# Kernel optimization log

Hardware: AMD Instinct MI355X
Metric: run time of the kernel (lower is better)

## Reference

```python
import jax, jax.numpy as jnp
import numpy as np
import math

NUM_HEADS = 8

def setup_inputs() -> dict:
    key = jax.random.key(0)
    k1, k2, k3 = jax.random.split(key, 3)
    B, N, C = 16, 4096, 512
    x = jax.random.normal(k1, (B, N, C), dtype=jnp.float32)
    qkv_w = jax.random.normal(k2, (3 * C, C), dtype=jnp.float32) * 0.02
    proj_w = jax.random.normal(k3, (C, C), dtype=jnp.float32) * 0.02
    proj_b = jnp.zeros((C,), dtype=jnp.float32)
    return {"x": x, "qkv_w": qkv_w, "proj_w": proj_w, "proj_b": proj_b}


def reference(x, qkv_w, proj_w, proj_b):
    # Attention with is_mask=1: row-wise windowed attention.
    B, N, C = x.shape
    H = W = int(math.isqrt(N))
    nh = NUM_HEADS
    hd = C // nh
    scale = hd ** (-0.5)

    # fold rows into batch: (B*H, W, C)
    img = x.reshape(B * H, W, C)
    # qkv linear (no bias): (B*H, W, 3C) -> (3, B*H, nh, W, hd)
    qkv = jnp.einsum('bwc,dc->bwd', img, qkv_w)
    qkv = qkv.reshape(B * H, W, 3, nh, hd).transpose(2, 0, 3, 1, 4)
    q, k, v = qkv[0], qkv[1], qkv[2]

    # scaled dot-product attention within each row window
    attn = jnp.einsum('bhqd,bhkd->bhqk', q, k) * scale
    attn = jax.nn.softmax(attn, axis=-1)
    out = jnp.einsum('bhqk,bhkd->bhqd', attn, v)   # (B*H, nh, W, hd)
    out = out.transpose(0, 2, 1, 3).reshape(B, N, C)

    # output projection
    return jnp.einsum('bnc,dc->bnd', out, proj_w) + proj_b
```

## Files before the change

### kernel.cpp

```cpp
#include <hip/hip_runtime.h>
#include <cstdint>
#include <cstddef>

typedef _Float16 half8 __attribute__((ext_vector_type(8)));
typedef _Float16 half4 __attribute__((ext_vector_type(4)));
typedef float f32x4 __attribute__((ext_vector_type(4)));

#define GLDS16(g, l) __builtin_amdgcn_global_load_lds( \
    (__attribute__((address_space(1))) void*)(g), \
    (__attribute__((address_space(3))) void*)(l), 16, 0, 0)

__global__ __launch_bounds__(256) void cvt_f32_f16(const float* __restrict__ src,
                                                   _Float16* __restrict__ dst, int n) {
  int i = (blockIdx.x * 256 + threadIdx.x) * 8;
  if (i >= n) return;
  float4 a = *(const float4*)(src + i);
  float4 b = *(const float4*)(src + i + 4);
  half8 h;
  h[0] = (_Float16)a.x; h[1] = (_Float16)a.y; h[2] = (_Float16)a.z; h[3] = (_Float16)a.w;
  h[4] = (_Float16)b.x; h[5] = (_Float16)b.y; h[6] = (_Float16)b.z; h[7] = (_Float16)b.w;
  *(half8*)(dst + i) = h;
}

template<int NOUT, int NT, bool BIAS>
__global__ __launch_bounds__(512, 2) void gemm_bt(const _Float16* __restrict__ A,
                                                  const _Float16* __restrict__ Bw,
                                                  const float* __restrict__ bias,
                                                  void* __restrict__ Cout) {
  constexpr int K = 512;
  constexpr int NIT = K / 32;
  __shared__ union {
    _Float16 S[3][2][8192];
    float E[2][16][264];
  } u;
  const int id  = blockIdx.x;
  const int xcd = id & 7;
  const int jj  = id >> 3;
  const int by  = (jj / NT) * 8 + xcd;
  const int bx  = jj % NT;
  const int m_base = by * 256, n_base = bx * 256;

  const int t    = threadIdx.x;
  const int lane = t & 63;
  const int wid  = t >> 6;
  const int wm   = wid & 1;
  const int wn   = wid >> 1;
  const int cl   = lane & 15, q = lane >> 4;

  f32x4 acc[8][4] = {};

  const int s0 = t, s1 = t + 512;
  const int r0 = ((s0 >> 6) << 4) | (s0 & 15), c0 = (s0 >> 4) & 3;
  const int r1 = ((s1 >> 6) << 4) | (s1 & 15), c1 = (s1 >> 4) & 3;
  const _Float16* a0 = A  + (size_t)(m_base + r0) * K + c0 * 8;
  const _Float16* a1 = A  + (size_t)(m_base + r1) * K + c1 * 8;
  const _Float16* b0 = Bw + (size_t)(n_base + r0) * K + c0 * 8;
  const _Float16* b1 = Bw + (size_t)(n_base + r1) * K + c1 * 8;

  const int lane8 = lane * 8;

  auto stage = [&](int kt, int b) {
    const int ko = kt * 32;
    GLDS16(a0 + ko, (char*)&u.S[b][0][0] + s0 * 16);
    GLDS16(a1 + ko, (char*)&u.S[b][0][0] + s1 * 16);
    GLDS16(b0 + ko, (char*)&u.S[b][1][0] + s0 * 16);
    GLDS16(b1 + ko, (char*)&u.S[b][1][0] + s1 * 16);
  };

  stage(0, 0);
  stage(1, 1);

#pragma unroll
  for (int k = 0; k < NIT; ++k) {
    if (k < NIT - 1) asm volatile("s_waitcnt vmcnt(4)" ::: "memory");
    else             asm volatile("s_waitcnt vmcnt(0)" ::: "memory");
    __builtin_amdgcn_s_barrier();
    asm volatile("" ::: "memory");
    if (k < NIT - 2) stage(k + 2, (k + 2) % 3);

    const _Float16* As = &u.S[k % 3][0][0];
    const _Float16* Bs = &u.S[k % 3][1][0];
    half8 af[8], bf[4];
#pragma unroll
    for (int i = 0; i < 8; i++) af[i] = *(const half8*)(As + (wm * 8 + i) * 512 + lane8);
#pragma unroll
    for (int i = 0; i < 4; i++) bf[i] = *(const half8*)(Bs + (wn * 4 + i) * 512 + lane8);
#pragma unroll
    for (int mt = 0; mt < 8; mt++)
#pragma unroll
      for (int nt = 0; nt < 4; nt++)
        acc[mt][nt] = __builtin_amdgcn_mfma_f32_16x16x32_f16(af[mt], bf[nt], acc[mt][nt], 0, 0, 0);
  }
  __syncthreads();

  const int eb = t >> 8;
  const int erow = (t >> 4) & 15;
  const int ecs = t & 15;
#pragma unroll
  for (int j = 0; j < 8; ++j) {
#pragma unroll
    for (int nt = 0; nt < 4; nt++)
#pragma unroll
      for (int r = 0; r < 4; r++)
        u.E[wm][q * 4 + r][wn * 64 + nt * 16 + cl] = acc[j][nt][r];
    __syncthreads();
    const size_t rg = (size_t)(m_base + (eb * 8 + j) * 16 + erow);
#pragma unroll
    for (int jo = 0; jo < 4; jo++) {
      const int cc = (ecs + 16 * jo) * 4;
      float4 e = *(const float4*)&u.E[eb][erow][cc];
      if constexpr (BIAS) {
        const float4 bb = *(const float4*)(bias + n_base + cc);
        e.x += bb.x; e.y += bb.y; e.z += bb.z; e.w += bb.w;
        *(float4*)((float*)Cout + rg * NOUT + n_base + cc) = e;
      } else {
        half4 hv;
        hv[0] = (_Float16)e.x; hv[1] = (_Float16)e.y;
        hv[2] = (_Float16)e.z; hv[3] = (_Float16)e.w;
        *(half4*)((_Float16*)Cout + rg * NOUT + n_base + cc) = hv;
      }
    }
    __syncthreads();
  }
}

__global__ __launch_bounds__(256, 3) void attn_win(const _Float16* __restrict__ QKV,
                                                   _Float16* __restrict__ Out) {
  __shared__ _Float16 Qs[4096];
  __shared__ _Float16 Ks[4096];
  __shared__ _Float16 Vt[64][72];
  __shared__ _Float16 Ps[64][72];
  __shared__ _Float16 Os[64][72];
  const int h = blockIdx.x, b = blockIdx.y;
  const int t = threadIdx.x;
  const int lane = t & 63, wid = t >> 6;
  const int cl = lane & 15, q = lane >> 4;

  {
    const int s0 = t, s1 = t + 256;
    const int r0 = ((s0 >> 7) << 4) | (s0 & 15), ch0 = (s0 >> 4) & 7;
    const int r1 = ((s1 >> 7) << 4) | (s1 & 15), ch1 = (s1 >> 4) & 7;
    const _Float16* g0 = QKV + (size_t)(b * 64 + r0) * 1536 + h * 64 + ch0 * 8;
    const _Float16* g1 = QKV + (size_t)(b * 64 + r1) * 1536 + h * 64 + ch1 * 8;
    GLDS16(g0,       (char*)Qs + s0 * 16);
    GLDS16(g1,       (char*)Qs + s1 * 16);
    GLDS16(g0 + 512, (char*)Ks + s0 * 16);
    GLDS16(g1 + 512, (char*)Ks + s1 * 16);

    const int vj = t & 63, vp = t >> 6;
    const _Float16* vsrc = QKV + (size_t)(b * 64 + vj) * 1536 + 1024 + h * 64 + vp * 16;
    half8 v0 = *(const half8*)vsrc;
    half8 v1 = *(const half8*)(vsrc + 8);
#pragma unroll
    for (int i = 0; i < 8; i++) Vt[vp * 16 + i][vj] = v0[i];
#pragma unroll
    for (int i = 0; i < 8; i++) Vt[vp * 16 + 8 + i][vj] = v1[i];
  }
  __syncthreads();

  const int m0 = wid * 16;
  const int lane8 = lane * 8;

  f32x4 s[4] = {};
#pragma unroll
  for (int ks = 0; ks < 2; ks++) {
    half8 a = *(const half8*)(Qs + wid * 1024 + ks * 512 + lane8);
#pragma unroll
    for (int nt = 0; nt < 4; nt++) {
      half8 bb = *(const half8*)(Ks + nt * 1024 + ks * 512 + lane8);
      s[nt] = __builtin_amdgcn_mfma_f32_16x16x32_f16(a, bb, s[nt], 0, 0, 0);
    }
  }

  constexpr float SC = 0.125f * 1.44269504088896340736f;
#pragma unroll
  for (int r = 0; r < 4; r++) {
    float mx = fmaxf(fmaxf(s[0][r], s[1][r]), fmaxf(s[2][r], s[3][r]));
    mx = fmaxf(mx, __shfl_xor(mx, 1));
    mx = fmaxf(mx, __shfl_xor(mx, 2));
    mx = fmaxf(mx, __shfl_xor(mx, 4));
    mx = fmaxf(mx, __shfl_xor(mx, 8));
    float e[4], ssum = 0.f;
#pragma unroll
    for (int nt = 0; nt < 4; nt++) { e[nt] = exp2f((s[nt][r] - mx) * SC); ssum += e[nt]; }
    ssum += __shfl_xor(ssum, 1);
    ssum += __shfl_xor(ssum, 2);
    ssum += __shfl_xor(ssum, 4);
    ssum += __shfl_xor(ssum, 8);
    float inv = 1.f / ssum;
    const int row = m0 + q * 4 + r;
#pragma unroll
    for (int nt = 0; nt < 4; nt++) Ps[row][nt * 16 + cl] = (_Float16)(e[nt] * inv);
  }
  __syncthreads();

  f32x4 o[4] = {};
#pragma unroll
  for (int ks = 0; ks < 2; ks++) {
    half8 a = *(const half8*)&Ps[m0 + cl][ks * 32 + q * 8];
#pragma unroll
    for (int nt = 0; nt < 4; nt++) {
      half8 bb = *(const half8*)&Vt[nt * 16 + cl][ks * 32 + q * 8];
      o[nt] = __builtin_amdgcn_mfma_f32_16x16x32_f16(a, bb, o[nt], 0, 0, 0);
    }
  }
#pragma unroll
  for (int nt = 0; nt < 4; nt++)
#pragma unroll
    for (int r = 0; r < 4; r++)
      Os[m0 + q * 4 + r][nt * 16 + cl] = (_Float16)o[nt][r];
  __syncthreads();

  {
    const int row = t >> 2, cs = t & 3;
    half8 h0 = *(const half8*)&Os[row][cs * 16];
    half8 h1 = *(const half8*)&Os[row][cs * 16 + 8];
    _Float16* dst = Out + (size_t)(b * 64 + row) * 512 + h * 64 + cs * 16;
    *(half8*)dst = h0;
    *((half8*)dst + 1) = h1;
  }
}

extern "C" void kernel_launch(void* const* d_in, const int* in_sizes, int n_in,
                              void* d_out, int out_size, void* d_ws, size_t ws_size,
                              hipStream_t stream) {
  const float* x      = (const float*)d_in[0];
  const float* qkv_w  = (const float*)d_in[1];
  const float* proj_w = (const float*)d_in[2];
  const float* proj_b = (const float*)d_in[3];
  float* out = (float*)d_out;

  char* ws = (char*)d_ws;
  _Float16* QKVh = (_Float16*)ws;
  _Float16* Xh   = (_Float16*)(ws + 201326592);
  _Float16* Outh = Xh;
  _Float16* Wq   = (_Float16*)(ws + 268435456);
  _Float16* Wp   = (_Float16*)(ws + 270008320);

  cvt_f32_f16<<<16384, 256, 0, stream>>>(x, Xh, 16 * 4096 * 512);
  cvt_f32_f16<<<384, 256, 0, stream>>>(qkv_w, Wq, 1536 * 512);
  cvt_f32_f16<<<128, 256, 0, stream>>>(proj_w, Wp, 512 * 512);
  gemm_bt<1536, 6, false><<<1536, 512, 0, stream>>>(Xh, Wq, nullptr, QKVh);
  attn_win<<<dim3(8, 1024), 256, 0, stream>>>(QKVh, Outh);
  gemm_bt<512, 2, true><<<512, 512, 0, stream>>>(Outh, Wp, proj_b, out);
}
```

Baseline: 480.0 us.

## Narrow GEMM tiles to 256x128, add setprio, and load Q directly into registers

The GEMM moves from 512-thread 256x256 tiles to 256-thread 256x128 tiles, which doubles the grid and cuts LDS per block. It also adds s_setprio around the MFMA loop, a trailing barrier per k-step, lgkmcnt-based barriers and a rotated epilogue read order to avoid LDS bank conflicts. The attention kernel drops the Q shared-memory buffer and loads Q fragments straight from global into registers, and its launch bound rises to 4 blocks per CU for occupancy. The cost is that B-tile reuse halves, since each A tile is now loaded for twice as many column blocks.

```diff
diff --git a/kernel.cpp b/kernel.cpp
--- a/kernel.cpp
+++ b/kernel.cpp
@@ -9,6 +9,9 @@
 #define GLDS16(g, l) __builtin_amdgcn_global_load_lds( \
     (__attribute__((address_space(1))) void*)(g), \
     (__attribute__((address_space(3))) void*)(l), 16, 0, 0)
+
+#define LBAR() do { asm volatile("s_waitcnt lgkmcnt(0)" ::: "memory"); \
+                    __builtin_amdgcn_s_barrier(); } while (0)
 
 __global__ __launch_bounds__(256) void cvt_f32_f16(const float* __restrict__ src,
                                                    _Float16* __restrict__ dst, int n) {
@@ -23,91 +26,105 @@
 }
 
 template<int NOUT, int NT, bool BIAS>
-__global__ __launch_bounds__(512, 2) void gemm_bt(const _Float16* __restrict__ A,
-                                                  const _Float16* __restrict__ Bw,
-                                                  const float* __restrict__ bias,
-                                                  void* __restrict__ Cout) {
+__global__ __launch_bounds__(256, 2) void gemm_wide(const _Float16* __restrict__ A,
+                                                    const _Float16* __restrict__ Bw,
+                                                    const float* __restrict__ bias,
+                                                    void* __restrict__ Cout) {
   constexpr int K = 512;
   constexpr int NIT = K / 32;
   __shared__ union {
-    _Float16 S[3][2][8192];
-    float E[2][16][264];
+    _Float16 S[3][12288];
+    float E[2][16][132];
   } u;
   const int id  = blockIdx.x;
   const int xcd = id & 7;
   const int jj  = id >> 3;
   const int by  = (jj / NT) * 8 + xcd;
   const int bx  = jj % NT;
-  const int m_base = by * 256, n_base = bx * 256;
+  const int m_base = by * 256, n_base = bx * 128;
 
   const int t    = threadIdx.x;
   const int lane = t & 63;
   const int wid  = t >> 6;
-  const int wm   = wid & 1;
-  const int wn   = wid >> 1;
+  const int wm   = wid >> 1;
+  const int wn   = wid & 1;
   const int cl   = lane & 15, q = lane >> 4;
 
   f32x4 acc[8][4] = {};
 
-  const int s0 = t, s1 = t + 512;
-  const int r0 = ((s0 >> 6) << 4) | (s0 & 15), c0 = (s0 >> 4) & 3;
-  const int r1 = ((s1 >> 6) << 4) | (s1 & 15), c1 = (s1 >> 4) & 3;
-  const _Float16* a0 = A  + (size_t)(m_base + r0) * K + c0 * 8;
-  const _Float16* a1 = A  + (size_t)(m_base + r1) * K + c1 * 8;
-  const _Float16* b0 = Bw + (size_t)(n_base + r0) * K + c0 * 8;
-  const _Float16* b1 = Bw + (size_t)(n_base + r1) * K + c1 * 8;
+  const _Float16* aP[4];
+  const _Float16* bP[2];
+#pragma unroll
+  for (int i = 0; i < 4; ++i) {
+    const int s = t + i * 256;
+    const int r = ((s >> 6) << 4) | (s & 15), ch = (s >> 4) & 3;
+    aP[i] = A + (size_t)(m_base + r) * K + ch * 8;
+  }
+#pragma unroll
+  for (int i = 0; i < 2; ++i) {
+    const int s = t + i * 256;
+    const int r = ((s >> 6) << 4) | (s & 15), ch = (s >> 4) & 3;
+    bP[i] = Bw + (size_t)(n_base + r) * K + ch * 8;
+  }
+  auto stage = [&](int kt) {
+    const int p = kt % 3;
+    const int ko = kt * 32;
+    char* base = (char*)&u.S[p][0];
+#pragma unroll
+    for (int i = 0; i < 4; ++i)
+      GLDS16(aP[i] + ko, base + (t + i * 256) * 16);
+#pragma unroll
+    for (int i = 0; i < 2; ++i)
+      GLDS16(bP[i] + ko, base + 16384 + (t + i * 256) * 16);
+  };
+
+  stage(0);
+  stage(1);
 
   const int lane8 = lane * 8;
-
-  auto stage = [&](int kt, int b) {
-    const int ko = kt * 32;
-    GLDS16(a0 + ko, (char*)&u.S[b][0][0] + s0 * 16);
-    GLDS16(a1 + ko, (char*)&u.S[b][0][0] + s1 * 16);
-    GLDS16(b0 + ko, (char*)&u.S[b][1][0] + s0 * 16);
-    GLDS16(b1 + ko, (char*)&u.S[b][1][0] + s1 * 16);
-  };
-
-  stage(0, 0);
-  stage(1, 1);
-
 #pragma unroll
   for (int k = 0; k < NIT; ++k) {
-    if (k < NIT - 1) asm volatile("s_waitcnt vmcnt(4)" ::: "memory");
+    if (k < NIT - 1) asm volatile("s_waitcnt vmcnt(6)" ::: "memory");
     else             asm volatile("s_waitcnt vmcnt(0)" ::: "memory");
     __builtin_amdgcn_s_barrier();
     asm volatile("" ::: "memory");
-    if (k < NIT - 2) stage(k + 2, (k + 2) % 3);
-
-    const _Float16* As = &u.S[k % 3][0][0];
-    const _Float16* Bs = &u.S[k % 3][1][0];
+    if (k + 2 < NIT) stage(k + 2);
+
+    const _Float16* As = &u.S[k % 3][0];
+    const _Float16* Bs = &u.S[k % 3][8192];
     half8 af[8], bf[4];
 #pragma unroll
-    for (int i = 0; i < 8; i++) af[i] = *(const half8*)(As + (wm * 8 + i) * 512 + lane8);
-#pragma unroll
-    for (int i = 0; i < 4; i++) bf[i] = *(const half8*)(Bs + (wn * 4 + i) * 512 + lane8);
-#pragma unroll
-    for (int mt = 0; mt < 8; mt++)
-#pragma unroll
-      for (int nt = 0; nt < 4; nt++)
-        acc[mt][nt] = __builtin_amdgcn_mfma_f32_16x16x32_f16(af[mt], bf[nt], acc[mt][nt], 0, 0, 0);
-  }
-  __syncthreads();
-
-  const int eb = t >> 8;
-  const int erow = (t >> 4) & 15;
-  const int ecs = t & 15;
+    for (int fm = 0; fm < 8; ++fm)
+      af[fm] = *(const half8*)(As + (wm * 8 + fm) * 512 + lane8);
+#pragma unroll
+    for (int fn = 0; fn < 4; ++fn)
+      bf[fn] = *(const half8*)(Bs + (wn * 4 + fn) * 512 + lane8);
+    __builtin_amdgcn_s_setprio(1);
+#pragma unroll
+    for (int fm = 0; fm < 8; ++fm)
+#pragma unroll
+      for (int fn = 0; fn < 4; ++fn)
+        acc[fm][fn] = __builtin_amdgcn_mfma_f32_16x16x32_f16(af[fm], bf[fn],
+                                                             acc[fm][fn], 0, 0, 0);
+    __builtin_amdgcn_s_setprio(0);
+    __builtin_amdgcn_s_barrier();
+  }
+  __syncthreads();
+
+  const int eb = t >> 7, erow = (t >> 3) & 15, ecs = t & 7;
 #pragma unroll
   for (int j = 0; j < 8; ++j) {
 #pragma unroll
-    for (int nt = 0; nt < 4; nt++)
-#pragma unroll
-      for (int r = 0; r < 4; r++)
-        u.E[wm][q * 4 + r][wn * 64 + nt * 16 + cl] = acc[j][nt][r];
-    __syncthreads();
-    const size_t rg = (size_t)(m_base + (eb * 8 + j) * 16 + erow);
-#pragma unroll
-    for (int jo = 0; jo < 4; jo++) {
-      const int cc = (ecs + 16 * jo) * 4;
+    for (int fn = 0; fn < 4; ++fn)
+#pragma unroll
+      for (int r = 0; r < 4; ++r)
+        u.E[wm][q * 4 + r][wn * 64 + fn * 16 + cl] = acc[j][fn][r];
+    LBAR();
+    const size_t rg = (size_t)(m_base + eb * 128 + j * 16 + erow);
+#pragma unroll
+    for (int jo = 0; jo < 4; ++jo) {
+      const int ch = ((ecs - erow) & 7) + 8 * jo;
+      const int cc = ch * 4;
       float4 e = *(const float4*)&u.E[eb][erow][cc];
       if constexpr (BIAS) {
         const float4 bb = *(const float4*)(bias + n_base + cc);
@@ -120,13 +137,12 @@
         *(half4*)((_Float16*)Cout + rg * NOUT + n_base + cc) = hv;
       }
     }
-    __syncthreads();
-  }
-}
-
-__global__ __launch_bounds__(256, 3) void attn_win(const _Float16* __restrict__ QKV,
+    LBAR();
+  }
+}
+
+__global__ __launch_bounds__(256, 4) void attn_win(const _Float16* __restrict__ QKV,
                                                    _Float16* __restrict__ Out) {
-  __shared__ _Float16 Qs[4096];
   __shared__ _Float16 Ks[4096];
   __shared__ _Float16 Vt[64][72];
   __shared__ _Float16 Ps[64][72];
@@ -135,17 +151,17 @@
   const int t = threadIdx.x;
   const int lane = t & 63, wid = t >> 6;
   const int cl = lane & 15, q = lane >> 4;
+  const int m0 = wid * 16;
+  const int lane8 = lane * 8;
 
   {
     const int s0 = t, s1 = t + 256;
     const int r0 = ((s0 >> 7) << 4) | (s0 & 15), ch0 = (s0 >> 4) & 7;
     const int r1 = ((s1 >> 7) << 4) | (s1 & 15), ch1 = (s1 >> 4) & 7;
-    const _Float16* g0 = QKV + (size_t)(b * 64 + r0) * 1536 + h * 64 + ch0 * 8;
-    const _Float16* g1 = QKV + (size_t)(b * 64 + r1) * 1536 + h * 64 + ch1 * 8;
-    GLDS16(g0,       (char*)Qs + s0 * 16);
-    GLDS16(g1,       (char*)Qs + s1 * 16);
-    GLDS16(g0 + 512, (char*)Ks + s0 * 16);
-    GLDS16(g1 + 512, (char*)Ks + s1 * 16);
+    const _Float16* g0 = QKV + (size_t)(b * 64 + r0) * 1536 + 512 + h * 64 + ch0 * 8;
+    const _Float16* g1 = QKV + (size_t)(b * 64 + r1) * 1536 + 512 + h * 64 + ch1 * 8;
+    GLDS16(g0, (char*)Ks + s0 * 16);
+    GLDS16(g1, (char*)Ks + s1 * 16);
 
     const int vj = t & 63, vp = t >> 6;
     const _Float16* vsrc = QKV + (size_t)(b * 64 + vj) * 1536 + 1024 + h * 64 + vp * 16;
@@ -156,20 +172,20 @@
 #pragma unroll
     for (int i = 0; i < 8; i++) Vt[vp * 16 + 8 + i][vj] = v1[i];
   }
-  __syncthreads();
-
-  const int m0 = wid * 16;
-  const int lane8 = lane * 8;
+
+  const _Float16* qsrc = QKV + (size_t)(b * 64 + m0 + cl) * 1536 + h * 64 + q * 8;
+  half8 qa0 = *(const half8*)qsrc;
+  half8 qa1 = *(const half8*)(qsrc + 32);
+
+  __syncthreads();
 
   f32x4 s[4] = {};
 #pragma unroll
-  for (int ks = 0; ks < 2; ks++) {
-    half8 a = *(const half8*)(Qs + wid * 1024 + ks * 512 + lane8);
-#pragma unroll
-    for (int nt = 0; nt < 4; nt++) {
-      half8 bb = *(const half8*)(Ks + nt * 1024 + ks * 512 + lane8);
-      s[nt] = __builtin_amdgcn_mfma_f32_16x16x32_f16(a, bb, s[nt], 0, 0, 0);
-    }
+  for (int nt = 0; nt < 4; nt++) {
+    half8 b0 = *(const half8*)(Ks + nt * 1024 + lane8);
+    half8 b1 = *(const half8*)(Ks + nt * 1024 + 512 + lane8);
+    s[nt] = __builtin_amdgcn_mfma_f32_16x16x32_f16(qa0, b0, s[nt], 0, 0, 0);
+    s[nt] = __builtin_amdgcn_mfma_f32_16x16x32_f16(qa1, b1, s[nt], 0, 0, 0);
   }
 
   constexpr float SC = 0.125f * 1.44269504088896340736f;
@@ -240,7 +256,7 @@
   cvt_f32_f16<<<16384, 256, 0, stream>>>(x, Xh, 16 * 4096 * 512);
   cvt_f32_f16<<<384, 256, 0, stream>>>(qkv_w, Wq, 1536 * 512);
   cvt_f32_f16<<<128, 256, 0, stream>>>(proj_w, Wp, 512 * 512);
-  gemm_bt<1536, 6, false><<<1536, 512, 0, stream>>>(Xh, Wq, nullptr, QKVh);
+  gemm_wide<1536, 12, false><<<3072, 256, 0, stream>>>(Xh, Wq, nullptr, QKVh);
   attn_win<<<dim3(8, 1024), 256, 0, stream>>>(QKVh, Outh);
-  gemm_bt<512, 2, true><<<512, 512, 0, stream>>>(Outh, Wp, proj_b, out);
-}
+  gemm_wide<512, 4, true><<<1024, 256, 0, stream>>>(Outh, Wp, proj_b, out);
+}
```

Measured after the change: 493.0 us. 2.7% more time.
